# Optimization experiments

Measured on AMD Instinct MI355X. Metric: run time of the kernel, lower is better.

## Reference

```python
import jax, jax.numpy as jnp
import numpy as np

EMBED_DIM = 1024
NUM_HEADS = 16
HEAD_DIM = EMBED_DIM // NUM_HEADS
B, S = 4, 2048


def setup_inputs() -> dict:
    key = jax.random.key(0)
    k1, k2, k3 = jax.random.split(key, 3)
    scale = 1.0 / np.sqrt(EMBED_DIM)
    x = jax.random.normal(k1, (B, S, EMBED_DIM), dtype=jnp.float32)
    W_qkv = jax.random.normal(k2, (EMBED_DIM, 3 * EMBED_DIM), dtype=jnp.float32) * scale
    b_qkv = jnp.zeros((3 * EMBED_DIM,), dtype=jnp.float32)
    W_out = jax.random.normal(k3, (EMBED_DIM, EMBED_DIM), dtype=jnp.float32) * scale
    b_out = jnp.zeros((EMBED_DIM,), dtype=jnp.float32)
    return {"x": x, "W_qkv": W_qkv, "b_qkv": b_qkv, "W_out": W_out, "b_out": b_out}


def reference(x, W_qkv, b_qkv, W_out, b_out):
    b, s, e = x.shape
    # fused QKV projection -> [b, s, 3, h, d]
    qkv = (x @ W_qkv + b_qkv).reshape(b, s, 3, NUM_HEADS, HEAD_DIM)
    qkv = jnp.transpose(qkv, (2, 0, 3, 1, 4))  # [3, b, h, s, d]
    q, k, v = qkv[0], qkv[1], qkv[2]
    scale = HEAD_DIM ** 0.5
    scores = jnp.einsum('bhqd,bhkd->bhqk', q, k) / scale  # [b, h, s, s]
    weights = jax.nn.softmax(scores, axis=-1)
    ctx = jnp.einsum('bhqk,bhkd->bhqd', weights, v)  # [b, h, s, d]
    ctx = jnp.transpose(ctx, (0, 2, 1, 3)).reshape(b, s, e)
    return ctx @ W_out + b_out
```

## Files before the change

### kernel.cpp

```cpp
#include <hip/hip_runtime.h>
#include <math.h>

#define B_ 4
#define S_ 2048
#define E_ 1024
#define H_ 16
#define D_ 64
#define M_TOT 8192
#define N_QKV 3072
#define K_ 1024

typedef __attribute__((ext_vector_type(8))) __bf16 bf16x8;
typedef __attribute__((ext_vector_type(2))) __bf16 bf16x2;
typedef __attribute__((ext_vector_type(8))) unsigned short u16x8;
typedef __attribute__((ext_vector_type(16))) float f32x16;

static __device__ __forceinline__ float bf2f(unsigned short u) {
  union { unsigned int u; float f; } x; x.u = ((unsigned int)u) << 16;
  return x.f;
}
static __device__ __forceinline__ unsigned int pack_bf16(float lo, float hi) {
  bf16x2 t; t[0] = (__bf16)lo; t[1] = (__bf16)hi;
  return __builtin_bit_cast(unsigned int, t);
}
static __device__ __forceinline__ void perm32swap(unsigned int& a, unsigned int& b) {
  asm volatile("v_permlane32_swap_b32 %0, %1" : "+v"(a), "+v"(b));
}

static __device__ __forceinline__ void gload16(const void* g, void* l) {
  __builtin_amdgcn_global_load_lds(
      (const __attribute__((address_space(1))) void*)g,
      (__attribute__((address_space(3))) void*)l, 16, 0, 0);
}

__global__ __launch_bounds__(256) void cvt_k(const float* __restrict__ in,
                                             unsigned short* __restrict__ out,
                                             int n8) {
  int i = blockIdx.x * 256 + threadIdx.x;
  if (i >= n8) return;
  float4 a = *reinterpret_cast<const float4*>(in + (size_t)i * 8);
  float4 b = *reinterpret_cast<const float4*>(in + (size_t)i * 8 + 4);
  uint4 o;
  o.x = pack_bf16(a.x, a.y); o.y = pack_bf16(a.z, a.w);
  o.z = pack_bf16(b.x, b.y); o.w = pack_bf16(b.z, b.w);
  *reinterpret_cast<uint4*>(out + (size_t)i * 8) = o;
}

__global__ __launch_bounds__(256) void tcvt_k(const float* __restrict__ in,
                                              unsigned short* __restrict__ out,
                                              int K, int N) {
  __shared__ float t[64][65];
  int n0 = blockIdx.x * 64, k0 = blockIdx.y * 64;
  int r = threadIdx.x >> 4, c = (threadIdx.x & 15) * 4;
#pragma unroll
  for (int it = 0; it < 4; ++it) {
    float4 v = *reinterpret_cast<const float4*>(&in[(size_t)(k0 + r + it * 16) * N + n0 + c]);
    t[r + it * 16][c + 0] = v.x; t[r + it * 16][c + 1] = v.y;
    t[r + it * 16][c + 2] = v.z; t[r + it * 16][c + 3] = v.w;
  }
  __syncthreads();
#pragma unroll
  for (int it = 0; it < 4; ++it) {
    int rr = r + it * 16;
    uint2 o;
    o.x = pack_bf16(t[c + 0][rr], t[c + 1][rr]);
    o.y = pack_bf16(t[c + 2][rr], t[c + 3][rr]);
    *reinterpret_cast<uint2*>(&out[(size_t)(n0 + rr) * K + k0 + c]) = o;
  }
}

template <int MODE>
__global__ __launch_bounds__(256) void gemm_k(
    const unsigned short* __restrict__ A, const unsigned short* __restrict__ BT,
    const float* __restrict__ bias, void* __restrict__ Cout) {
  __shared__ __attribute__((aligned(128))) char lds[2][24576];
  const int tid = threadIdx.x;
  const int wv = tid >> 6, lane = tid & 63;
  const int ln = lane & 31, hh = lane >> 5;
  const int m0 = blockIdx.y * 128, n0 = blockIdx.x * 256;
  const int r4 = lane >> 2, slot = lane & 3;

  const char* Ab = (const char*)A;
  const char* Bb = (const char*)BT;
  size_t a_off[2], b_off[4];
#pragma unroll
  for (int i = 0; i < 2; ++i) {
    int r = wv * 32 + i * 16 + r4;
    a_off[i] = (size_t)(m0 + r) * (K_ * 2) + (size_t)((slot ^ ((r >> 1) & 3)) * 16);
  }
#pragma unroll
  for (int j = 0; j < 4; ++j) {
    int r = wv * 64 + j * 16 + r4;
    b_off[j] = (size_t)(n0 + r) * (K_ * 2) + (size_t)((slot ^ ((r >> 1) & 3)) * 16);
  }

  f32x16 acc[4][2];
#pragma unroll
  for (int gr = 0; gr < 4; ++gr)
#pragma unroll
    for (int gc = 0; gc < 2; ++gc)
#pragma unroll
      for (int e = 0; e < 16; ++e) acc[gr][gc][e] = 0.f;

#define STAGE(dst, tt)                                                        \
  do {                                                                        \
    char* _d = (dst);                                                         \
    size_t _ko = (size_t)(tt) * 64;                                           \
    _Pragma("unroll") for (int i = 0; i < 2; ++i)                             \
        gload16(Ab + a_off[i] + _ko, _d + (wv * 32 + i * 16) * 64);           \
    _Pragma("unroll") for (int j = 0; j < 4; ++j)                             \
        gload16(Bb + b_off[j] + _ko, _d + 8192 + (wv * 64 + j * 16) * 64);    \
  } while (0)

  STAGE(&lds[0][0], 0);
  __syncthreads();
  for (int t = 0; t < K_ / 32; ++t) {
    char* cur = &lds[t & 1][0];
    char* nxt = &lds[(t + 1) & 1][0];
    if (t + 1 < K_ / 32) STAGE(nxt, t + 1);
#pragma unroll
    for (int s = 0; s < 2; ++s) {
      const int cb = s * 32 + hh * 16;
      bf16x8 af[4], bfr[2];
#pragma unroll
      for (int gr = 0; gr < 4; ++gr) {
        int row = gr * 32 + ln;
        af[gr] = *reinterpret_cast<const bf16x8*>(
            cur + row * 64 + (cb ^ (((row >> 1) & 3) << 4)));
      }
#pragma unroll
      for (int gc = 0; gc < 2; ++gc) {
        int row = wv * 64 + gc * 32 + ln;
        bfr[gc] = *reinterpret_cast<const bf16x8*>(
            cur + 8192 + row * 64 + (cb ^ (((row >> 1) & 3) << 4)));
      }
#pragma unroll
      for (int gr = 0; gr < 4; ++gr)
#pragma unroll
        for (int gc = 0; gc < 2; ++gc)
          acc[gr][gc] = __builtin_amdgcn_mfma_f32_32x32x16_bf16(
              af[gr], bfr[gc], acc[gr][gc], 0, 0, 0);
    }
    __syncthreads();
  }
#undef STAGE

  const int ncol0 = n0 + wv * 64;
  if (MODE == 0) {
    unsigned short* qkv = (unsigned short*)Cout;
#pragma unroll
    for (int gc = 0; gc < 2; ++gc) {
      int n = ncol0 + gc * 32 + ln;
      float bv = bias[n];
      int which = n >> 10, h = (n >> 6) & 15, d = n & 63;
      unsigned short* base =
          qkv + (((size_t)which * B_ * H_ + h) * S_) * D_ + d;
#pragma unroll
      for (int gr = 0; gr < 4; ++gr)
#pragma unroll
        for (int r = 0; r < 16; r += 2) {
          int m = m0 + gr * 32 + 4 * hh + (r & 3) + 8 * (r >> 2);
          unsigned int w = pack_bf16(acc[gr][gc][r] + bv, acc[gr][gc][r + 1] + bv);
          int bi = m >> 11, si = m & 2047;
          size_t off = ((size_t)bi * H_ * S_ + si) * D_;
          base[off] = (unsigned short)w;
          base[off + D_] = (unsigned short)(w >> 16);
        }
    }
  } else {
    float* out = (float*)Cout;
#pragma unroll
    for (int gc = 0; gc < 2; ++gc) {
      int n = ncol0 + gc * 32 + ln;
      float bv = bias[n];
#pragma unroll
      for (int gr = 0; gr < 4; ++gr)
#pragma unroll
        for (int r = 0; r < 16; ++r) {
          int m = m0 + gr * 32 + 4 * hh + (r & 3) + 8 * (r >> 2);
          out[(size_t)m * E_ + n] = acc[gr][gc][r] + bv;
        }
    }
  }
}

__global__ __launch_bounds__(256, 4) void attn_k(
    const unsigned short* __restrict__ qkv, unsigned short* __restrict__ ctx) {
  __shared__ unsigned short lds[2][4096];
  const int tid = threadIdx.x;
  const int wv = tid >> 6;
  const int lane = tid & 63;
  const int ln = lane & 31;
  const int hh = lane >> 5;
  const int q0 = blockIdx.x * 128;
  const int bh = blockIdx.y;
  const int b = bh >> 4, head = bh & 15;
  const size_t SZ = (size_t)B_ * H_ * S_ * D_;
  const size_t plane = ((size_t)b * H_ + head) * (size_t)S_ * D_;
  const unsigned short* Qp = qkv + plane;
  const unsigned short* Kp = qkv + SZ + plane;
  const unsigned short* Vp = qkv + 2 * SZ + plane;

  const float SC = 0.125f * 1.4426950408889634f;
  const int qrow = q0 + wv * 32 + ln;
  bf16x8 qf[4];
#pragma unroll
  for (int db = 0; db < 4; ++db) {
    u16x8 qr = *reinterpret_cast<const u16x8*>(Qp + (size_t)qrow * D_ + db * 16 + hh * 8);
    bf16x8 qs;
#pragma unroll
    for (int j = 0; j < 8; ++j) qs[j] = (__bf16)(bf2f(qr[j]) * SC);
    qf[db] = qs;
  }

  const int krow = tid >> 3, kg = tid & 7;
  const int vk = tid & 31, vd0 = (tid >> 5) * 8;
  const int kwoff = (krow * 128 + kg * 16) ^ ((krow & 7) << 4);
  char* lbA = (char*)&lds[0][0];
  char* lbB = (char*)&lds[1][0];

  {
    u16x8 kr = *reinterpret_cast<const u16x8*>(Kp + (size_t)krow * D_ + kg * 8);
    u16x8 vr = *reinterpret_cast<const u16x8*>(Vp + (size_t)vk * D_ + vd0);
    *reinterpret_cast<u16x8*>(lbA + kwoff) = kr;
#pragma unroll
    for (int i = 0; i < 8; ++i) {
      int d = vd0 + i;
      *reinterpret_cast<unsigned short*>(lbA + 4096 + ((d * 64 + vk * 2) ^ ((d & 7) << 4))) = vr[i];
    }
  }
  __syncthreads();

  f32x16 acc0, acc1;
#pragma unroll
  for (int e = 0; e < 16; ++e) { acc0[e] = 0.f; acc1[e] = 0.f; }
  float mrun = -1e30f, lrun = 0.f;

  for (int t = 0; t < 64; ++t) {
    char* cur = (t & 1) ? lbB : lbA;
    char* nxt = (t & 1) ? lbA : lbB;
    const bool more = (t + 1 < 64);
    u16x8 krn, vrn;
    if (more) {
      int k0n = (t + 1) * 32;
      krn = *reinterpret_cast<const u16x8*>(Kp + (size_t)(k0n + krow) * D_ + kg * 8);
      vrn = *reinterpret_cast<const u16x8*>(Vp + (size_t)(k0n + vk) * D_ + vd0);
    }
    f32x16 st;
#pragma unroll
    for (int e = 0; e < 16; ++e) st[e] = 0.f;
#pragma unroll
    for (int db = 0; db < 4; ++db) {
      bf16x8 kf = *reinterpret_cast<const bf16x8*>(
          cur + ((ln * 128 + db * 32 + hh * 16) ^ ((ln & 7) << 4)));
      st = __builtin_amdgcn_mfma_f32_32x32x16_bf16(kf, qf[db], st, 0, 0, 0);
    }
    float ta = fmaxf(fmaxf(st[0], st[1]), st[2]);
    float tb = fmaxf(fmaxf(st[3], st[4]), st[5]);
    float tc = fmaxf(fmaxf(st[6], st[7]), st[8]);
    float td = fmaxf(fmaxf(st[9], st[10]), st[11]);
    float te = fmaxf(fmaxf(st[12], st[13]), st[14]);
    float tm = fmaxf(fmaxf(fmaxf(ta, tb), fmaxf(tc, td)), fmaxf(te, st[15]));
    tm = fmaxf(tm, __shfl_xor(tm, 32, 64));
    if (!__all(tm <= mrun + 8.0f)) {
      float newm = fmaxf(mrun, tm);
      float alpha = exp2f(mrun - newm);
      mrun = newm;
      lrun *= alpha;
      acc0 *= alpha;
      acc1 *= alpha;
    }
    float p[16];
#pragma unroll
    for (int r = 0; r < 16; ++r) p[r] = exp2f(st[r] - mrun);
    float s0 = (p[0] + p[1]) + (p[2] + p[3]);
    float s1 = (p[4] + p[5]) + (p[6] + p[7]);
    float s2 = (p[8] + p[9]) + (p[10] + p[11]);
    float s3 = (p[12] + p[13]) + (p[14] + p[15]);
    float psum = (s0 + s1) + (s2 + s3);
    psum += __shfl_xor(psum, 32, 64);
    lrun += psum;
    unsigned int w0 = pack_bf16(p[0], p[1]);
    unsigned int w1 = pack_bf16(p[2], p[3]);
    unsigned int w2 = pack_bf16(p[4], p[5]);
    unsigned int w3 = pack_bf16(p[6], p[7]);
    unsigned int w4 = pack_bf16(p[8], p[9]);
    unsigned int w5 = pack_bf16(p[10], p[11]);
    unsigned int w6 = pack_bf16(p[12], p[13]);
    unsigned int w7 = pack_bf16(p[14], p[15]);
    perm32swap(w0, w2);
    perm32swap(w1, w3);
    perm32swap(w4, w6);
    perm32swap(w5, w7);
    uint4 fw0 = make_uint4(w0, w1, w2, w3);
    uint4 fw1 = make_uint4(w4, w5, w6, w7);
    bf16x8 pb0 = __builtin_bit_cast(bf16x8, fw0);
    bf16x8 pb1 = __builtin_bit_cast(bf16x8, fw1);
    {
      int vd = ln;
      bf16x8 va = *reinterpret_cast<const bf16x8*>(
          cur + 4096 + ((vd * 64 + hh * 16) ^ ((vd & 7) << 4)));
      bf16x8 vb = *reinterpret_cast<const bf16x8*>(
          cur + 4096 + ((vd * 64 + 32 + hh * 16) ^ ((vd & 7) << 4)));
      acc0 = __builtin_amdgcn_mfma_f32_32x32x16_bf16(va, pb0, acc0, 0, 0, 0);
      acc0 = __builtin_amdgcn_mfma_f32_32x32x16_bf16(vb, pb1, acc0, 0, 0, 0);
    }
    {
      int vd = ln + 32;
      bf16x8 va = *reinterpret_cast<const bf16x8*>(
          cur + 4096 + ((vd * 64 + hh * 16) ^ ((vd & 7) << 4)));
      bf16x8 vb = *reinterpret_cast<const bf16x8*>(
          cur + 4096 + ((vd * 64 + 32 + hh * 16) ^ ((vd & 7) << 4)));
      acc1 = __builtin_amdgcn_mfma_f32_32x32x16_bf16(va, pb0, acc1, 0, 0, 0);
      acc1 = __builtin_amdgcn_mfma_f32_32x32x16_bf16(vb, pb1, acc1, 0, 0, 0);
    }
    if (more) {
      *reinterpret_cast<u16x8*>(nxt + kwoff) = krn;
#pragma unroll
      for (int i = 0; i < 8; ++i) {
        int d = vd0 + i;
        *reinterpret_cast<unsigned short*>(nxt + 4096 + ((d * 64 + vk * 2) ^ ((d & 7) << 4))) = vrn[i];
      }
    }
    __syncthreads();
  }

  float invl = 1.0f / lrun;
  unsigned short* orow = ctx + ((size_t)b * S_ + qrow) * E_ + head * D_;
#pragma unroll
  for (int g = 0; g < 4; ++g) {
    int d0 = 8 * g + 4 * hh;
    uint2 o0, o1;
    o0.x = pack_bf16(acc0[4 * g + 0] * invl, acc0[4 * g + 1] * invl);
    o0.y = pack_bf16(acc0[4 * g + 2] * invl, acc0[4 * g + 3] * invl);
    o1.x = pack_bf16(acc1[4 * g + 0] * invl, acc1[4 * g + 1] * invl);
    o1.y = pack_bf16(acc1[4 * g + 2] * invl, acc1[4 * g + 3] * invl);
    *reinterpret_cast<uint2*>(orow + d0) = o0;
    *reinterpret_cast<uint2*>(orow + d0 + 32) = o1;
  }
}

extern "C" void kernel_launch(void* const* d_in, const int* in_sizes, int n_in,
                              void* d_out, int out_size, void* d_ws, size_t ws_size,
                              hipStream_t stream) {
  const float* x    = (const float*)d_in[0];
  const float* Wqkv = (const float*)d_in[1];
  const float* bqkv = (const float*)d_in[2];
  const float* Wout = (const float*)d_in[3];
  const float* bout = (const float*)d_in[4];
  float* out = (float*)d_out;

  char* ws = (char*)d_ws;
  unsigned short* qkv_b = (unsigned short*)ws;                     ws += (size_t)3 * B_ * H_ * S_ * D_ * 2;
  unsigned short* ctx_b = (unsigned short*)ws;                     ws += (size_t)M_TOT * E_ * 2;
  unsigned short* xb    = (unsigned short*)ws;                     ws += (size_t)M_TOT * E_ * 2;
  unsigned short* wqT   = (unsigned short*)ws;                     ws += (size_t)N_QKV * K_ * 2;
  unsigned short* woT   = (unsigned short*)ws;

  cvt_k<<<dim3(M_TOT * E_ / 8 / 256), 256, 0, stream>>>(x, xb, M_TOT * E_ / 8);
  tcvt_k<<<dim3(N_QKV / 64, K_ / 64), 256, 0, stream>>>(Wqkv, wqT, K_, N_QKV);
  tcvt_k<<<dim3(E_ / 64, K_ / 64), 256, 0, stream>>>(Wout, woT, K_, E_);

  gemm_k<0><<<dim3(N_QKV / 256, M_TOT / 128), 256, 0, stream>>>(xb, wqT, bqkv, qkv_b);
  attn_k<<<dim3(S_ / 128, B_ * H_), 256, 0, stream>>>(qkv_b, ctx_b);
  gemm_k<1><<<dim3(E_ / 256, M_TOT / 128), 256, 0, stream>>>(ctx_b, woT, bout, out);
}
```

Baseline: 238.9 us.

## Write V transposed from QKV GEMM and stage attention tiles via direct LDS loads

The QKV GEMM epilogue now writes V in a [b,h,d,s] transposed layout with packed 8-byte stores, replacing the scattered per-element stores. The attention kernel uses this layout to copy K and V tiles straight into LDS with 16-byte global-to-LDS loads on a swizzled source address, instead of staging through registers and scattering V element by element. It also hoists the V fragment reads ahead of the softmax and adds s_setprio around the MFMA groups. The cost is an extra workspace buffer and a dependence on the gload16 helper and the new swizzle being consistent.

```diff
diff --git a/kernel.cpp b/kernel.cpp
--- a/kernel.cpp
+++ b/kernel.cpp
@@ -72,7 +72,8 @@
 template <int MODE>
 __global__ __launch_bounds__(256) void gemm_k(
     const unsigned short* __restrict__ A, const unsigned short* __restrict__ BT,
-    const float* __restrict__ bias, void* __restrict__ Cout) {
+    const float* __restrict__ bias, void* __restrict__ Cout,
+    unsigned short* __restrict__ vT) {
   __shared__ __attribute__((aligned(128))) char lds[2][24576];
   const int tid = threadIdx.x;
   const int wv = tid >> 6, lane = tid & 63;
@@ -153,19 +154,34 @@
       int n = ncol0 + gc * 32 + ln;
       float bv = bias[n];
       int which = n >> 10, h = (n >> 6) & 15, d = n & 63;
-      unsigned short* base =
-          qkv + (((size_t)which * B_ * H_ + h) * S_) * D_ + d;
-#pragma unroll
-      for (int gr = 0; gr < 4; ++gr)
-#pragma unroll
-        for (int r = 0; r < 16; r += 2) {
-          int m = m0 + gr * 32 + 4 * hh + (r & 3) + 8 * (r >> 2);
-          unsigned int w = pack_bf16(acc[gr][gc][r] + bv, acc[gr][gc][r + 1] + bv);
-          int bi = m >> 11, si = m & 2047;
-          size_t off = ((size_t)bi * H_ * S_ + si) * D_;
-          base[off] = (unsigned short)w;
-          base[off + D_] = (unsigned short)(w >> 16);
-        }
+      if (which < 2) {
+        unsigned short* base =
+            qkv + (((size_t)which * B_ * H_ + h) * S_) * D_ + d;
+#pragma unroll
+        for (int gr = 0; gr < 4; ++gr)
+#pragma unroll
+          for (int r = 0; r < 16; r += 2) {
+            int m = m0 + gr * 32 + 4 * hh + (r & 3) + 8 * (r >> 2);
+            unsigned int w = pack_bf16(acc[gr][gc][r] + bv, acc[gr][gc][r + 1] + bv);
+            int bi = m >> 11, si = m & 2047;
+            size_t off = ((size_t)bi * H_ * S_ + si) * D_;
+            base[off] = (unsigned short)w;
+            base[off + D_] = (unsigned short)(w >> 16);
+          }
+      } else {
+        unsigned short* vbase = vT + ((size_t)h * D_ + d) * S_;
+#pragma unroll
+        for (int gr = 0; gr < 4; ++gr)
+#pragma unroll
+          for (int rq = 0; rq < 4; ++rq) {
+            int mb = m0 + gr * 32 + 4 * hh + 8 * rq;
+            int bi = mb >> 11, si = mb & 2047;
+            uint2 w;
+            w.x = pack_bf16(acc[gr][gc][rq * 4 + 0] + bv, acc[gr][gc][rq * 4 + 1] + bv);
+            w.y = pack_bf16(acc[gr][gc][rq * 4 + 2] + bv, acc[gr][gc][rq * 4 + 3] + bv);
+            *reinterpret_cast<uint2*>(vbase + (size_t)bi * H_ * D_ * S_ + si) = w;
+          }
+      }
     }
   } else {
     float* out = (float*)Cout;
@@ -185,8 +201,9 @@
 }
 
 __global__ __launch_bounds__(256, 4) void attn_k(
-    const unsigned short* __restrict__ qkv, unsigned short* __restrict__ ctx) {
-  __shared__ unsigned short lds[2][4096];
+    const unsigned short* __restrict__ qkv, const unsigned short* __restrict__ vT,
+    unsigned short* __restrict__ ctx) {
+  __shared__ __attribute__((aligned(128))) char lds[2][8192];
   const int tid = threadIdx.x;
   const int wv = tid >> 6;
   const int lane = tid & 63;
@@ -199,7 +216,7 @@
   const size_t plane = ((size_t)b * H_ + head) * (size_t)S_ * D_;
   const unsigned short* Qp = qkv + plane;
   const unsigned short* Kp = qkv + SZ + plane;
-  const unsigned short* Vp = qkv + 2 * SZ + plane;
+  const unsigned short* Vp = vT + ((size_t)b * H_ + head) * (size_t)D_ * S_;
 
   const float SC = 0.125f * 1.4426950408889634f;
   const int qrow = q0 + wv * 32 + ln;
@@ -213,54 +230,53 @@
     qf[db] = qs;
   }
 
-  const int krow = tid >> 3, kg = tid & 7;
-  const int vk = tid & 31, vd0 = (tid >> 5) * 8;
-  const int kwoff = (krow * 128 + kg * 16) ^ ((krow & 7) << 4);
-  char* lbA = (char*)&lds[0][0];
-  char* lbB = (char*)&lds[1][0];
-
-  {
-    u16x8 kr = *reinterpret_cast<const u16x8*>(Kp + (size_t)krow * D_ + kg * 8);
-    u16x8 vr = *reinterpret_cast<const u16x8*>(Vp + (size_t)vk * D_ + vd0);
-    *reinterpret_cast<u16x8*>(lbA + kwoff) = kr;
-#pragma unroll
-    for (int i = 0; i < 8; ++i) {
-      int d = vd0 + i;
-      *reinterpret_cast<unsigned short*>(lbA + 4096 + ((d * 64 + vk * 2) ^ ((d & 7) << 4))) = vr[i];
-    }
-  }
+  const size_t ksrc = (size_t)(tid >> 3) * 64 +
+                      (size_t)(((tid & 7) ^ ((tid >> 3) & 7)) * 8);
+  const size_t vsrc = (size_t)(tid >> 2) * S_ +
+                      (size_t)(((tid & 3) ^ ((tid >> 3) & 3)) * 8);
+
+#define ASTAGE(bsel, tt)                                                      \
+  do {                                                                        \
+    char* _d = &lds[(bsel)][0];                                               \
+    gload16(Kp + (size_t)(tt) * 2048 + ksrc, _d + tid * 16);                  \
+    gload16(Vp + (size_t)(tt) * 32 + vsrc, _d + 4096 + tid * 16);             \
+  } while (0)
+
+  ASTAGE(0, 0);
   __syncthreads();
 
   f32x16 acc0, acc1;
 #pragma unroll
   for (int e = 0; e < 16; ++e) { acc0[e] = 0.f; acc1[e] = 0.f; }
   float mrun = -1e30f, lrun = 0.f;
+  const int xo = (ln >> 1) & 3;
 
   for (int t = 0; t < 64; ++t) {
-    char* cur = (t & 1) ? lbB : lbA;
-    char* nxt = (t & 1) ? lbA : lbB;
-    const bool more = (t + 1 < 64);
-    u16x8 krn, vrn;
-    if (more) {
-      int k0n = (t + 1) * 32;
-      krn = *reinterpret_cast<const u16x8*>(Kp + (size_t)(k0n + krow) * D_ + kg * 8);
-      vrn = *reinterpret_cast<const u16x8*>(Vp + (size_t)(k0n + vk) * D_ + vd0);
-    }
+    const int cb = t & 1;
+    if (t + 1 < 64) ASTAGE(cb ^ 1, t + 1);
+    const char* cur = &lds[cb][0];
     f32x16 st;
 #pragma unroll
     for (int e = 0; e < 16; ++e) st[e] = 0.f;
+    __builtin_amdgcn_s_setprio(1);
 #pragma unroll
     for (int db = 0; db < 4; ++db) {
       bf16x8 kf = *reinterpret_cast<const bf16x8*>(
-          cur + ((ln * 128 + db * 32 + hh * 16) ^ ((ln & 7) << 4)));
+          cur + ln * 128 + ((((db << 1) | hh) ^ (ln & 7)) << 4));
       st = __builtin_amdgcn_mfma_f32_32x32x16_bf16(kf, qf[db], st, 0, 0, 0);
     }
-    float ta = fmaxf(fmaxf(st[0], st[1]), st[2]);
-    float tb = fmaxf(fmaxf(st[3], st[4]), st[5]);
-    float tc = fmaxf(fmaxf(st[6], st[7]), st[8]);
-    float td = fmaxf(fmaxf(st[9], st[10]), st[11]);
-    float te = fmaxf(fmaxf(st[12], st[13]), st[14]);
-    float tm = fmaxf(fmaxf(fmaxf(ta, tb), fmaxf(tc, td)), fmaxf(te, st[15]));
+    __builtin_amdgcn_s_setprio(0);
+    const char* vb_ = cur + 4096;
+    bf16x8 vA = *reinterpret_cast<const bf16x8*>(vb_ + ln * 64 + ((hh ^ xo) << 4));
+    bf16x8 vB = *reinterpret_cast<const bf16x8*>(vb_ + ln * 64 + (((2 + hh) ^ xo) << 4));
+    bf16x8 vC = *reinterpret_cast<const bf16x8*>(vb_ + (ln + 32) * 64 + ((hh ^ xo) << 4));
+    bf16x8 vD = *reinterpret_cast<const bf16x8*>(vb_ + (ln + 32) * 64 + (((2 + hh) ^ xo) << 4));
+    float m1 = fmaxf(fmaxf(st[0], st[1]), st[2]);
+    float m2 = fmaxf(fmaxf(st[3], st[4]), st[5]);
+    float m3 = fmaxf(fmaxf(st[6], st[7]), st[8]);
+    float m4 = fmaxf(fmaxf(st[9], st[10]), st[11]);
+    float m5 = fmaxf(fmaxf(st[12], st[13]), st[14]);
+    float tm = fmaxf(fmaxf(fmaxf(m1, m2), fmaxf(m3, m4)), fmaxf(m5, st[15]));
     tm = fmaxf(tm, __shfl_xor(tm, 32, 64));
     if (!__all(tm <= mrun + 8.0f)) {
       float newm = fmaxf(mrun, tm);
@@ -292,38 +308,17 @@
     perm32swap(w1, w3);
     perm32swap(w4, w6);
     perm32swap(w5, w7);
-    uint4 fw0 = make_uint4(w0, w1, w2, w3);
-    uint4 fw1 = make_uint4(w4, w5, w6, w7);
-    bf16x8 pb0 = __builtin_bit_cast(bf16x8, fw0);
-    bf16x8 pb1 = __builtin_bit_cast(bf16x8, fw1);
-    {
-      int vd = ln;
-      bf16x8 va = *reinterpret_cast<const bf16x8*>(
-          cur + 4096 + ((vd * 64 + hh * 16) ^ ((vd & 7) << 4)));
-      bf16x8 vb = *reinterpret_cast<const bf16x8*>(
-          cur + 4096 + ((vd * 64 + 32 + hh * 16) ^ ((vd & 7) << 4)));
-      acc0 = __builtin_amdgcn_mfma_f32_32x32x16_bf16(va, pb0, acc0, 0, 0, 0);
-      acc0 = __builtin_amdgcn_mfma_f32_32x32x16_bf16(vb, pb1, acc0, 0, 0, 0);
-    }
-    {
-      int vd = ln + 32;
-      bf16x8 va = *reinterpret_cast<const bf16x8*>(
-          cur + 4096 + ((vd * 64 + hh * 16) ^ ((vd & 7) << 4)));
-      bf16x8 vb = *reinterpret_cast<const bf16x8*>(
-          cur + 4096 + ((vd * 64 + 32 + hh * 16) ^ ((vd & 7) << 4)));
-      acc1 = __builtin_amdgcn_mfma_f32_32x32x16_bf16(va, pb0, acc1, 0, 0, 0);
-      acc1 = __builtin_amdgcn_mfma_f32_32x32x16_bf16(vb, pb1, acc1, 0, 0, 0);
-    }
-    if (more) {
-      *reinterpret_cast<u16x8*>(nxt + kwoff) = krn;
-#pragma unroll
-      for (int i = 0; i < 8; ++i) {
-        int d = vd0 + i;
-        *reinterpret_cast<unsigned short*>(nxt + 4096 + ((d * 64 + vk * 2) ^ ((d & 7) << 4))) = vrn[i];
-      }
-    }
+    bf16x8 pb0 = __builtin_bit_cast(bf16x8, make_uint4(w0, w1, w2, w3));
+    bf16x8 pb1 = __builtin_bit_cast(bf16x8, make_uint4(w4, w5, w6, w7));
+    __builtin_amdgcn_s_setprio(1);
+    acc0 = __builtin_amdgcn_mfma_f32_32x32x16_bf16(vA, pb0, acc0, 0, 0, 0);
+    acc0 = __builtin_amdgcn_mfma_f32_32x32x16_bf16(vB, pb1, acc0, 0, 0, 0);
+    acc1 = __builtin_amdgcn_mfma_f32_32x32x16_bf16(vC, pb0, acc1, 0, 0, 0);
+    acc1 = __builtin_amdgcn_mfma_f32_32x32x16_bf16(vD, pb1, acc1, 0, 0, 0);
+    __builtin_amdgcn_s_setprio(0);
     __syncthreads();
   }
+#undef ASTAGE
 
   float invl = 1.0f / lrun;
   unsigned short* orow = ctx + ((size_t)b * S_ + qrow) * E_ + head * D_;
@@ -351,17 +346,18 @@
   float* out = (float*)d_out;
 
   char* ws = (char*)d_ws;
-  unsigned short* qkv_b = (unsigned short*)ws;                     ws += (size_t)3 * B_ * H_ * S_ * D_ * 2;
-  unsigned short* ctx_b = (unsigned short*)ws;                     ws += (size_t)M_TOT * E_ * 2;
-  unsigned short* xb    = (unsigned short*)ws;                     ws += (size_t)M_TOT * E_ * 2;
-  unsigned short* wqT   = (unsigned short*)ws;                     ws += (size_t)N_QKV * K_ * 2;
+  unsigned short* qkv_b = (unsigned short*)ws;  ws += (size_t)2 * B_ * H_ * S_ * D_ * 2;
+  unsigned short* vT_b  = (unsigned short*)ws;  ws += (size_t)B_ * H_ * D_ * S_ * 2;
+  unsigned short* ctx_b = (unsigned short*)ws;  ws += (size_t)M_TOT * E_ * 2;
+  unsigned short* xb    = (unsigned short*)ws;  ws += (size_t)M_TOT * E_ * 2;
+  unsigned short* wqT   = (unsigned short*)ws;  ws += (size_t)N_QKV * K_ * 2;
   unsigned short* woT   = (unsigned short*)ws;
 
   cvt_k<<<dim3(M_TOT * E_ / 8 / 256), 256, 0, stream>>>(x, xb, M_TOT * E_ / 8);
   tcvt_k<<<dim3(N_QKV / 64, K_ / 64), 256, 0, stream>>>(Wqkv, wqT, K_, N_QKV);
   tcvt_k<<<dim3(E_ / 64, K_ / 64), 256, 0, stream>>>(Wout, woT, K_, E_);
 
-  gemm_k<0><<<dim3(N_QKV / 256, M_TOT / 128), 256, 0, stream>>>(xb, wqT, bqkv, qkv_b);
-  attn_k<<<dim3(S_ / 128, B_ * H_), 256, 0, stream>>>(qkv_b, ctx_b);
-  gemm_k<1><<<dim3(E_ / 256, M_TOT / 128), 256, 0, stream>>>(ctx_b, woT, bout, out);
-}
+  gemm_k<0><<<dim3(N_QKV / 256, M_TOT / 128), 256, 0, stream>>>(xb, wqT, bqkv, qkv_b, vT_b);
+  attn_k<<<dim3(S_ / 128, B_ * H_), 256, 0, stream>>>(qkv_b, vT_b, ctx_b);
+  gemm_k<1><<<dim3(E_ / 256, M_TOT / 128), 256, 0, stream>>>(ctx_b, woT, bout, out, nullptr);
+}
```

Measured after the change: 245.7 us. +2.8%, slower.
